# Performance work log

Hardware: AMD Instinct MI355X
Metric: run time of the kernel (lower is better)

Reference implementation:

```python
import jax, jax.numpy as jnp
import numpy as np

B, T, C = 4, 1024, 1024
N_HEAD = 16
MEMORY = 64  # sliding-window size: key j visible to query i iff 0 <= i-j <= MEMORY


def setup_inputs() -> dict:
    key = jax.random.key(0)
    k1, k2, k3 = jax.random.split(key, 3)
    x = jax.random.normal(k1, (B, T, C), dtype=jnp.float32)
    # torch Linear weight is [out, in]; we store transposed [in, out] for x @ W
    W_attn = jax.random.normal(k2, (C, 3 * C), dtype=jnp.float32) * (1.0 / np.sqrt(C))
    W_proj = jax.random.normal(k3, (C, C), dtype=jnp.float32) * (1.0 / np.sqrt(C))
    return {"x": x, "W_attn": W_attn, "W_proj": W_proj}


def reference(x, W_attn, W_proj):
    Bv, Tv, Cv = x.shape
    hd = Cv // N_HEAD
    qkv = x @ W_attn                               # [B,T,3C]
    q, k, v = jnp.split(qkv, 3, axis=-1)
    def heads(t):
        return t.reshape(Bv, Tv, N_HEAD, hd).transpose(0, 2, 1, 3)  # [B,H,T,hd]
    q, k, v = heads(q), heads(k), heads(v)
    scale = 1.0 / np.sqrt(hd)
    scores = jnp.einsum('bhqd,bhkd->bhqk', q, k) * scale            # [B,H,T,T]
    i = jnp.arange(Tv)
    diff = i[:, None] - i[None, :]                                  # i - j
    band_mask = (diff >= 0) & (diff <= MEMORY)                      # M1 * ~M2
    y = jax.nn.softmax(jnp.where(band_mask, scores, -jnp.inf), axis=-1) @ v
    # get_att=True path: full causal attention probabilities (no window)
    att = jax.nn.softmax(jnp.where(diff >= 0, scores, -jnp.inf), axis=-1)
    att_std = jnp.std(att, axis=0, ddof=1)                          # torch .std default ddof=1
    y = y.transpose(0, 2, 1, 3).reshape(Bv, Tv, Cv)
    y = y @ W_proj
    return (y, att, att_std)
```

## Files before the change

### kernel.cpp

```cpp
#include <hip/hip_runtime.h>
#include <hip/hip_bf16.h>
#include <stdint.h>

#define Bb 4
#define Tt 1024
#define Hh 16
#define HD 64
#define C3 3072
#define WIN 64

typedef __bf16 bf16x8 __attribute__((ext_vector_type(8)));
typedef float f32x4 __attribute__((ext_vector_type(4)));

#define MFMA16(a, b, c) __builtin_amdgcn_mfma_f32_16x16x32_bf16((a), (b), (c), 0, 0, 0)

static __device__ __forceinline__ unsigned short f2bf(float f) {
  union { float f; unsigned u; } v; v.f = f;
  unsigned r = (v.u + 0x7FFFu + ((v.u >> 16) & 1u)) >> 16;
  return (unsigned short)r;
}
static __device__ __forceinline__ float bf2f(unsigned short h) {
  union { unsigned u; float f; } v; v.u = ((unsigned)h) << 16;
  return v.f;
}

__global__ __launch_bounds__(256) void k_prep(const float* __restrict__ x,
                                              const float* __restrict__ Wa,
                                              const float* __restrict__ Wp,
                                              unsigned short* __restrict__ xbf,
                                              unsigned short* __restrict__ WtA,
                                              unsigned short* __restrict__ WtP) {
  __shared__ float tile[32][33];
  const int blk = blockIdx.x;
  const int tid = threadIdx.x;
  if (blk < 4096) {
    int i = blk * 256 + tid;
    float4 v = ((const float4*)x)[i];
    ushort4 o;
    o.x = f2bf(v.x); o.y = f2bf(v.y); o.z = f2bf(v.z); o.w = f2bf(v.w);
    ((ushort4*)xbf)[i] = o;
    return;
  }
  const float* Win; unsigned short* Wt; int N, n0, k0;
  if (blk < 7168) { int bb = blk - 4096; Win = Wa; Wt = WtA; N = 3072; n0 = (bb % 96) * 32; k0 = (bb / 96) * 32; }
  else           { int bb = blk - 7168; Win = Wp; Wt = WtP; N = 1024; n0 = (bb % 32) * 32; k0 = (bb / 32) * 32; }
  const int K = 1024;
  int tx = tid & 31, ty = tid >> 5;
  for (int r = ty; r < 32; r += 8)
    tile[r][tx] = Win[(size_t)(k0 + r) * N + n0 + tx];
  __syncthreads();
  for (int r = ty; r < 32; r += 8)
    Wt[(size_t)(n0 + r) * K + k0 + tx] = f2bf(tile[tx][r]);
}

template <int BM, int BF16_OUT, int SCALEQ>
__global__ __launch_bounds__(256) void k_gemm_bt(const unsigned short* __restrict__ A,
                                                 const unsigned short* __restrict__ Bt,
                                                 void* __restrict__ Cv, int M, int N, int K) {
  constexpr int MI = BM / 32;
  __shared__ unsigned short lds[BM * 32 + 128 * 32];
  unsigned short* as_ = lds;
  unsigned short* bs_ = lds + BM * 32;
  const int tid = threadIdx.x;
  const int m0 = blockIdx.x * BM, n0 = blockIdx.y * 128;
  const int w = tid >> 6, lane = tid & 63;
  const int wm = (w >> 1) * (BM / 2), wn = (w & 1) * 64;
  const int lrow = lane & 15, lk = lane >> 4;

  f32x4 z = {0.f, 0.f, 0.f, 0.f};
  f32x4 acc[MI][4];
#pragma unroll
  for (int i = 0; i < MI; ++i)
#pragma unroll
    for (int j = 0; j < 4; ++j) acc[i][j] = z;

  const int nk = K >> 5;
  for (int kt = 0; kt < nk; ++kt) {
    const int k0 = kt << 5;
    __syncthreads();
#pragma unroll
    for (int p = 0; p < BM / 64; ++p) {
      int seg = tid + p * 256;
      int row = seg >> 2, ks = (seg & 3) << 3;
      __builtin_amdgcn_global_load_lds(
          (__attribute__((address_space(1))) void*)(A + (size_t)(m0 + row) * K + k0 + ks),
          (__attribute__((address_space(3))) void*)(as_ + seg * 8), 16, 0, 0);
    }
#pragma unroll
    for (int p = 0; p < 2; ++p) {
      int seg = tid + p * 256;
      int row = seg >> 2, ks = (seg & 3) << 3;
      __builtin_amdgcn_global_load_lds(
          (__attribute__((address_space(1))) void*)(Bt + (size_t)(n0 + row) * K + k0 + ks),
          (__attribute__((address_space(3))) void*)(bs_ + seg * 8), 16, 0, 0);
    }
    __syncthreads();
    bf16x8 af[MI], bfr[4];
#pragma unroll
    for (int f = 0; f < MI; ++f)
      af[f] = *(const bf16x8*)(as_ + (wm + f * 16 + lrow) * 32 + lk * 8);
#pragma unroll
    for (int f = 0; f < 4; ++f)
      bfr[f] = *(const bf16x8*)(bs_ + (wn + f * 16 + lrow) * 32 + lk * 8);
#pragma unroll
    for (int i = 0; i < MI; ++i)
#pragma unroll
      for (int j = 0; j < 4; ++j) acc[i][j] = MFMA16(af[i], bfr[j], acc[i][j]);
  }
  const int r0 = lk * 4;
#pragma unroll
  for (int i = 0; i < MI; ++i)
#pragma unroll
    for (int j = 0; j < 4; ++j)
#pragma unroll
      for (int r = 0; r < 4; ++r) {
        int gm = m0 + wm + i * 16 + r0 + r;
        int gn = n0 + wn + j * 16 + lrow;
        float v = acc[i][j][r];
        if (SCALEQ) {
          if (gn < 1024) v *= 0.125f;
        }
        if (BF16_OUT)
          ((unsigned short*)Cv)[(size_t)gm * N + gn] = f2bf(v);
        else
          ((float*)Cv)[(size_t)gm * N + gn] = v;
      }
}

__global__ __launch_bounds__(256) void k_att(const unsigned short* __restrict__ qkv,
                                             float* __restrict__ att, float* __restrict__ astd) {
  const int ti = 31 - blockIdx.x;
  const int h = blockIdx.y;
  const int i0 = ti * 32;
  const int tid = threadIdx.x;
  const int w = tid >> 6, lane = tid & 63;
  const int lrow = lane & 15, lk = lane >> 4;

  __shared__ float smr[4][32][2];
  __shared__ float wbuf[4][32][36];

  {
    const int b1 = w;
    const size_t qb_ = ((size_t)(b1 * Tt + i0 + lrow)) * C3 + h * 64 + lk * 8;
    bf16x8 q00 = *(const bf16x8*)(qkv + qb_);
    bf16x8 q01 = *(const bf16x8*)(qkv + qb_ + 32);
    bf16x8 q10 = *(const bf16x8*)(qkv + qb_ + (size_t)16 * C3);
    bf16x8 q11 = *(const bf16x8*)(qkv + qb_ + (size_t)16 * C3 + 32);

    float m[2][4], l[2][4];
#pragma unroll
    for (int i2 = 0; i2 < 2; ++i2)
#pragma unroll
      for (int r = 0; r < 4; ++r) { m[i2][r] = -1e30f; l[i2][r] = 0.f; }

    for (int jt = 0; jt <= ti; ++jt) {
      const int j0 = jt * 32;
      const size_t krowa = ((size_t)(b1 * Tt + j0 + lrow)) * C3 + 1024 + h * 64 + lk * 8;
      const size_t krowb = krowa + (size_t)16 * C3;
      bf16x8 k00 = *(const bf16x8*)(qkv + krowa);
      bf16x8 k01 = *(const bf16x8*)(qkv + krowa + 32);
      bf16x8 k10 = *(const bf16x8*)(qkv + krowb);
      bf16x8 k11 = *(const bf16x8*)(qkv + krowb + 32);
      const int ja = j0 + lrow, jb2 = j0 + 16 + lrow;
#pragma unroll
      for (int i2 = 0; i2 < 2; ++i2) {
        bf16x8 qa = i2 ? q10 : q00;
        bf16x8 qb = i2 ? q11 : q01;
        f32x4 sa = {0.f, 0.f, 0.f, 0.f}, sb = {0.f, 0.f, 0.f, 0.f};
        sa = MFMA16(qa, k00, sa);
        sa = MFMA16(qb, k01, sa);
        sb = MFMA16(qa, k10, sb);
        sb = MFMA16(qb, k11, sb);
#pragma unroll
        for (int r = 0; r < 4; ++r) {
          int ig = i0 + i2 * 16 + lk * 4 + r;
          int oka = (ja <= ig), okb = (jb2 <= ig);
          float va = oka ? sa[r] : -1e30f;
          float vb = okb ? sb[r] : -1e30f;
          float mn = fmaxf(m[i2][r], fmaxf(va, vb));
          float pa = oka ? __expf(sa[r] - mn) : 0.f;
          float pb = okb ? __expf(sb[r] - mn) : 0.f;
          l[i2][r] = l[i2][r] * __expf(m[i2][r] - mn) + pa + pb;
          m[i2][r] = mn;
        }
      }
    }
#pragma unroll
    for (int i2 = 0; i2 < 2; ++i2)
#pragma unroll
      for (int r = 0; r < 4; ++r) {
        float mm = m[i2][r], ll = l[i2][r];
#pragma unroll
        for (int d = 1; d <= 8; d <<= 1) {
          float mo = __shfl_xor(mm, d);
          float lo = __shfl_xor(ll, d);
          float mn = fmaxf(mm, mo);
          ll = ll * __expf(mm - mn) + lo * __expf(mo - mn);
          mm = mn;
        }
        if (lrow == 0) {
          int row = i2 * 16 + lk * 4 + r;
          smr[b1][row][0] = mm;
          smr[b1][row][1] = 1.0f / ll;
        }
      }
  }
  __syncthreads();

  bf16x8 qf[4][2][2];
#pragma unroll
  for (int b = 0; b < 4; ++b) {
    const size_t qb_ = ((size_t)(b * Tt + i0 + lrow)) * C3 + h * 64 + lk * 8;
    qf[b][0][0] = *(const bf16x8*)(qkv + qb_);
    qf[b][0][1] = *(const bf16x8*)(qkv + qb_ + 32);
    qf[b][1][0] = *(const bf16x8*)(qkv + qb_ + (size_t)16 * C3);
    qf[b][1][1] = *(const bf16x8*)(qkv + qb_ + (size_t)16 * C3 + 32);
  }

  const float4 z4 = make_float4(0.f, 0.f, 0.f, 0.f);
  for (int jt = w; jt < 32; jt += 4) {
    const int j0 = jt * 32;
    if (jt > ti) {
#pragma unroll
      for (int b = 0; b < 4; ++b)
#pragma unroll
        for (int q = 0; q < 4; ++q) {
          int f = q * 64 + lane;
          int row = f >> 3, c4 = f & 7;
          *(float4*)&att[(((size_t)(b * Hh + h)) * Tt + i0 + row) * Tt + j0 + c4 * 4] = z4;
        }
#pragma unroll
      for (int q = 0; q < 4; ++q) {
        int f = q * 64 + lane;
        int row = f >> 3, c4 = f & 7;
        *(float4*)&astd[((size_t)h * Tt + i0 + row) * Tt + j0 + c4 * 4] = z4;
      }
      continue;
    }
    float s1[2][2][4], s2[2][2][4];
#pragma unroll
    for (int i2 = 0; i2 < 2; ++i2)
#pragma unroll
      for (int j2 = 0; j2 < 2; ++j2)
#pragma unroll
        for (int r = 0; r < 4; ++r) { s1[i2][j2][r] = 0.f; s2[i2][j2][r] = 0.f; }

#pragma unroll
    for (int b = 0; b < 4; ++b) {
      const size_t krowa = ((size_t)(b * Tt + j0 + lrow)) * C3 + 1024 + h * 64 + lk * 8;
      const size_t krowb = krowa + (size_t)16 * C3;
      bf16x8 k00 = *(const bf16x8*)(qkv + krowa);
      bf16x8 k01 = *(const bf16x8*)(qkv + krowa + 32);
      bf16x8 k10 = *(const bf16x8*)(qkv + krowb);
      bf16x8 k11 = *(const bf16x8*)(qkv + krowb + 32);
#pragma unroll
      for (int i2 = 0; i2 < 2; ++i2) {
        float mm[4], rr[4];
#pragma unroll
        for (int r = 0; r < 4; ++r) {
          int row = i2 * 16 + lk * 4 + r;
          mm[r] = smr[b][row][0];
          rr[r] = smr[b][row][1];
        }
#pragma unroll
        for (int j2 = 0; j2 < 2; ++j2) {
          f32x4 s = {0.f, 0.f, 0.f, 0.f};
          s = MFMA16(qf[b][i2][0], j2 ? k10 : k00, s);
          s = MFMA16(qf[b][i2][1], j2 ? k11 : k01, s);
          const int jg2 = j0 + j2 * 16 + lrow;
#pragma unroll
          for (int r = 0; r < 4; ++r) {
            int ig = i0 + i2 * 16 + lk * 4 + r;
            float p = (jg2 <= ig) ? __expf(s[r] - mm[r]) * rr[r] : 0.f;
            wbuf[w][i2 * 16 + lk * 4 + r][j2 * 16 + lrow] = p;
            s1[i2][j2][r] += p;
            s2[i2][j2][r] += p * p;
          }
        }
      }
#pragma unroll
      for (int q = 0; q < 4; ++q) {
        int f = q * 64 + lane;
        int row = f >> 3, c4 = f & 7;
        float4 v = *(float4*)&wbuf[w][row][c4 * 4];
        *(float4*)&att[(((size_t)(b * Hh + h)) * Tt + i0 + row) * Tt + j0 + c4 * 4] = v;
      }
    }
#pragma unroll
    for (int i2 = 0; i2 < 2; ++i2)
#pragma unroll
      for (int j2 = 0; j2 < 2; ++j2)
#pragma unroll
        for (int r = 0; r < 4; ++r) {
          float mean = s1[i2][j2][r] * 0.25f;
          float var = (s2[i2][j2][r] - 4.f * mean * mean) * (1.f / 3.f);
          wbuf[w][i2 * 16 + lk * 4 + r][j2 * 16 + lrow] = sqrtf(fmaxf(var, 0.f));
        }
#pragma unroll
    for (int q = 0; q < 4; ++q) {
      int f = q * 64 + lane;
      int row = f >> 3, c4 = f & 7;
      float4 v = *(float4*)&wbuf[w][row][c4 * 4];
      *(float4*)&astd[((size_t)h * Tt + i0 + row) * Tt + j0 + c4 * 4] = v;
    }
  }
}

__global__ __launch_bounds__(256) void k_bandy(const unsigned short* __restrict__ qkv,
                                               unsigned short* __restrict__ yh) {
  __shared__ unsigned short qls[64 * 66];
  __shared__ unsigned short kls[128 * 66];
  __shared__ unsigned short vls[128 * 66];
  __shared__ float pls[4][80];

  int blk = blockIdx.x;
  int it = blk & 15, h = (blk >> 4) & 15, b = blk >> 8;
  int i0 = it * 64;
  int jb = i0 - 64;
  int tid = threadIdx.x;

  for (int r = tid; r < 320; r += 256) {
    unsigned short* dst;
    int grow, sel;
    if (r < 64) { dst = qls + r * 66; grow = i0 + r; sel = 0; }
    else if (r < 192) { dst = kls + (r - 64) * 66; grow = jb + (r - 64); sel = 1; }
    else { dst = vls + (r - 192) * 66; grow = jb + (r - 192); sel = 2; }
    if (grow < 0) {
      for (int t = 0; t < 32; ++t) ((unsigned*)dst)[t] = 0u;
    } else {
      const unsigned* src = (const unsigned*)(qkv + ((size_t)(b * Tt + grow)) * C3 + sel * 1024 + h * 64);
      for (int t = 0; t < 32; ++t) ((unsigned*)dst)[t] = src[t];
    }
  }
  __syncthreads();

  const int w = tid >> 6, lane = tid & 63;
  for (int rr = 0; rr < 16; ++rr) {
    const int i = i0 + (w << 4) + rr;
    const int io = i - i0;
    const int ja = i - 64 + lane;
    const unsigned* qrow = (const unsigned*)(qls + io * 66);
    const unsigned* krow = (const unsigned*)(kls + (size_t)(io + lane) * 66);
    const unsigned* kerow = (const unsigned*)(kls + (size_t)(io + 64) * 66);
    float sa = 0.f, se = 0.f;
#pragma unroll 8
    for (int t = 0; t < 32; ++t) {
      unsigned qq = qrow[t];
      float q0 = bf2f((unsigned short)qq), q1 = bf2f((unsigned short)(qq >> 16));
      unsigned kk = krow[t];
      sa = fmaf(q0, bf2f((unsigned short)kk), sa);
      sa = fmaf(q1, bf2f((unsigned short)(kk >> 16)), sa);
      unsigned ke = kerow[t];
      se = fmaf(q0, bf2f((unsigned short)ke), se);
      se = fmaf(q1, bf2f((unsigned short)(ke >> 16)), se);
    }
    if (ja < 0) sa = -1e30f;
    float m = sa;
    m = fmaxf(m, __shfl_xor(m, 1));
    m = fmaxf(m, __shfl_xor(m, 2));
    m = fmaxf(m, __shfl_xor(m, 4));
    m = fmaxf(m, __shfl_xor(m, 8));
    m = fmaxf(m, __shfl_xor(m, 16));
    m = fmaxf(m, __shfl_xor(m, 32));
    m = fmaxf(m, se);
    float pa = __expf(sa - m);
    float pe = __expf(se - m);
    float sum = pa;
    sum += __shfl_xor(sum, 1);
    sum += __shfl_xor(sum, 2);
    sum += __shfl_xor(sum, 4);
    sum += __shfl_xor(sum, 8);
    sum += __shfl_xor(sum, 16);
    sum += __shfl_xor(sum, 32);
    sum += pe;
    float rl = 1.0f / sum;
    pls[w][lane] = pa * rl;
    if (lane == 0) pls[w][64] = pe * rl;
    float y = 0.f;
#pragma unroll 4
    for (int t = 0; t <= 64; ++t)
      y = fmaf(pls[w][t], bf2f(vls[(size_t)(io + t) * 66 + lane]), y);
    yh[((size_t)(b * Tt + i)) * 1024 + h * 64 + lane] = f2bf(y);
  }
}

extern "C" void kernel_launch(void* const* d_in, const int* in_sizes, int n_in,
                              void* d_out, int out_size, void* d_ws, size_t ws_size,
                              hipStream_t stream) {
  const float* x = (const float*)d_in[0];
  const float* Wa = (const float*)d_in[1];
  const float* Wp = (const float*)d_in[2];

  float* out = (float*)d_out;
  float* y_out = out;
  float* att = out + (size_t)4194304;
  float* astd = out + (size_t)71303168;

  char* ws = (char*)d_ws;
  unsigned short* qkv = (unsigned short*)ws;
  unsigned short* yh = (unsigned short*)(ws + 25165824);
  unsigned short* WtP = (unsigned short*)(ws + 33554432);

  char* yreg = (char*)d_out;
  unsigned short* WtA = (unsigned short*)yreg;
  unsigned short* xbf = (unsigned short*)(yreg + 6291456);

  k_prep<<<8192, 256, 0, stream>>>(x, Wa, Wp, xbf, WtA, WtP);
  k_gemm_bt<128, 1, 1><<<dim3(32, 24), 256, 0, stream>>>(xbf, WtA, qkv, 4096, 3072, 1024);
  k_att<<<dim3(32, 16), 256, 0, stream>>>(qkv, att, astd);
  k_bandy<<<1024, 256, 0, stream>>>(qkv, yh);
  k_gemm_bt<64, 0, 0><<<dim3(64, 8), 256, 0, stream>>>(yh, WtP, y_out, 4096, 1024, 1024);
}
```

Measured before the change: 293.0 us.

## Merge causal-attention and band-attention kernels into one interleaved launch

Combines the full causal attention probability/std kernel and the sliding-window band attention kernel into a single launch. Block IDs are interleaved so that one of every three blocks does causal-attention work and the other two do band work, letting the two independent workloads share the GPU at the same time. The intent is to fill idle compute units during the imbalanced, memory-heavy att kernel and to remove one launch boundary. The cost is a shared memory allocation sized to the larger of the two paths, which can lower occupancy for the band blocks, and a divergent kernel body that may increase register pressure.

```diff
diff --git a/kernel.cpp b/kernel.cpp
--- a/kernel.cpp
+++ b/kernel.cpp
@@ -127,260 +127,264 @@
       }
 }
 
-__global__ __launch_bounds__(256) void k_att(const unsigned short* __restrict__ qkv,
-                                             float* __restrict__ att, float* __restrict__ astd) {
-  const int ti = 31 - blockIdx.x;
-  const int h = blockIdx.y;
-  const int i0 = ti * 32;
+__global__ __launch_bounds__(256) void k_attband(const unsigned short* __restrict__ qkv,
+                                                 float* __restrict__ att, float* __restrict__ astd,
+                                                 unsigned short* __restrict__ yh) {
+  __shared__ __align__(16) char smem[43520];
+  const int bid = blockIdx.x;
+  const int g = bid / 3, rsel = bid - g * 3;
   const int tid = threadIdx.x;
   const int w = tid >> 6, lane = tid & 63;
-  const int lrow = lane & 15, lk = lane >> 4;
-
-  __shared__ float smr[4][32][2];
-  __shared__ float wbuf[4][32][36];
-
-  {
-    const int b1 = w;
-    const size_t qb_ = ((size_t)(b1 * Tt + i0 + lrow)) * C3 + h * 64 + lk * 8;
-    bf16x8 q00 = *(const bf16x8*)(qkv + qb_);
-    bf16x8 q01 = *(const bf16x8*)(qkv + qb_ + 32);
-    bf16x8 q10 = *(const bf16x8*)(qkv + qb_ + (size_t)16 * C3);
-    bf16x8 q11 = *(const bf16x8*)(qkv + qb_ + (size_t)16 * C3 + 32);
-
-    float m[2][4], l[2][4];
-#pragma unroll
-    for (int i2 = 0; i2 < 2; ++i2)
-#pragma unroll
-      for (int r = 0; r < 4; ++r) { m[i2][r] = -1e30f; l[i2][r] = 0.f; }
-
-    for (int jt = 0; jt <= ti; ++jt) {
+
+  if (rsel == 0) {
+    const int ti = 31 - (g & 31);
+    const int h = g >> 5;
+    const int i0 = ti * 32;
+    const int lrow = lane & 15, lk = lane >> 4;
+    float (*smr)[32][2] = (float(*)[32][2])smem;
+    float (*wbuf)[32][36] = (float(*)[32][36])(smem + 1024);
+
+    {
+      const int b1 = w;
+      const size_t qb_ = ((size_t)(b1 * Tt + i0 + lrow)) * C3 + h * 64 + lk * 8;
+      bf16x8 q00 = *(const bf16x8*)(qkv + qb_);
+      bf16x8 q01 = *(const bf16x8*)(qkv + qb_ + 32);
+      bf16x8 q10 = *(const bf16x8*)(qkv + qb_ + (size_t)16 * C3);
+      bf16x8 q11 = *(const bf16x8*)(qkv + qb_ + (size_t)16 * C3 + 32);
+
+      float m[2][4], l[2][4];
+#pragma unroll
+      for (int i2 = 0; i2 < 2; ++i2)
+#pragma unroll
+        for (int r = 0; r < 4; ++r) { m[i2][r] = -1e30f; l[i2][r] = 0.f; }
+
+      for (int jt = 0; jt <= ti; ++jt) {
+        const int j0 = jt * 32;
+        const size_t krowa = ((size_t)(b1 * Tt + j0 + lrow)) * C3 + 1024 + h * 64 + lk * 8;
+        const size_t krowb = krowa + (size_t)16 * C3;
+        bf16x8 k00 = *(const bf16x8*)(qkv + krowa);
+        bf16x8 k01 = *(const bf16x8*)(qkv + krowa + 32);
+        bf16x8 k10 = *(const bf16x8*)(qkv + krowb);
+        bf16x8 k11 = *(const bf16x8*)(qkv + krowb + 32);
+        const int ja = j0 + lrow, jb2 = j0 + 16 + lrow;
+#pragma unroll
+        for (int i2 = 0; i2 < 2; ++i2) {
+          bf16x8 qa = i2 ? q10 : q00;
+          bf16x8 qb = i2 ? q11 : q01;
+          f32x4 sa = {0.f, 0.f, 0.f, 0.f}, sb = {0.f, 0.f, 0.f, 0.f};
+          sa = MFMA16(qa, k00, sa);
+          sa = MFMA16(qb, k01, sa);
+          sb = MFMA16(qa, k10, sb);
+          sb = MFMA16(qb, k11, sb);
+#pragma unroll
+          for (int r = 0; r < 4; ++r) {
+            int ig = i0 + i2 * 16 + lk * 4 + r;
+            int oka = (ja <= ig), okb = (jb2 <= ig);
+            float va = oka ? sa[r] : -1e30f;
+            float vb = okb ? sb[r] : -1e30f;
+            float mn = fmaxf(m[i2][r], fmaxf(va, vb));
+            float pa = oka ? __expf(sa[r] - mn) : 0.f;
+            float pb = okb ? __expf(sb[r] - mn) : 0.f;
+            l[i2][r] = l[i2][r] * __expf(m[i2][r] - mn) + pa + pb;
+            m[i2][r] = mn;
+          }
+        }
+      }
+#pragma unroll
+      for (int i2 = 0; i2 < 2; ++i2)
+#pragma unroll
+        for (int r = 0; r < 4; ++r) {
+          float mm = m[i2][r], ll = l[i2][r];
+#pragma unroll
+          for (int d = 1; d <= 8; d <<= 1) {
+            float mo = __shfl_xor(mm, d);
+            float lo = __shfl_xor(ll, d);
+            float mn = fmaxf(mm, mo);
+            ll = ll * __expf(mm - mn) + lo * __expf(mo - mn);
+            mm = mn;
+          }
+          if (lrow == 0) {
+            int row = i2 * 16 + lk * 4 + r;
+            smr[b1][row][0] = mm;
+            smr[b1][row][1] = 1.0f / ll;
+          }
+        }
+    }
+    __syncthreads();
+
+    bf16x8 qf[4][2][2];
+#pragma unroll
+    for (int b = 0; b < 4; ++b) {
+      const size_t qb_ = ((size_t)(b * Tt + i0 + lrow)) * C3 + h * 64 + lk * 8;
+      qf[b][0][0] = *(const bf16x8*)(qkv + qb_);
+      qf[b][0][1] = *(const bf16x8*)(qkv + qb_ + 32);
+      qf[b][1][0] = *(const bf16x8*)(qkv + qb_ + (size_t)16 * C3);
+      qf[b][1][1] = *(const bf16x8*)(qkv + qb_ + (size_t)16 * C3 + 32);
+    }
+
+    const float4 z4 = make_float4(0.f, 0.f, 0.f, 0.f);
+    for (int jt = w; jt < 32; jt += 4) {
       const int j0 = jt * 32;
-      const size_t krowa = ((size_t)(b1 * Tt + j0 + lrow)) * C3 + 1024 + h * 64 + lk * 8;
-      const size_t krowb = krowa + (size_t)16 * C3;
-      bf16x8 k00 = *(const bf16x8*)(qkv + krowa);
-      bf16x8 k01 = *(const bf16x8*)(qkv + krowa + 32);
-      bf16x8 k10 = *(const bf16x8*)(qkv + krowb);
-      bf16x8 k11 = *(const bf16x8*)(qkv + krowb + 32);
-      const int ja = j0 + lrow, jb2 = j0 + 16 + lrow;
-#pragma unroll
-      for (int i2 = 0; i2 < 2; ++i2) {
-        bf16x8 qa = i2 ? q10 : q00;
-        bf16x8 qb = i2 ? q11 : q01;
-        f32x4 sa = {0.f, 0.f, 0.f, 0.f}, sb = {0.f, 0.f, 0.f, 0.f};
-        sa = MFMA16(qa, k00, sa);
-        sa = MFMA16(qb, k01, sa);
-        sb = MFMA16(qa, k10, sb);
-        sb = MFMA16(qb, k11, sb);
-#pragma unroll
-        for (int r = 0; r < 4; ++r) {
-          int ig = i0 + i2 * 16 + lk * 4 + r;
-          int oka = (ja <= ig), okb = (jb2 <= ig);
-          float va = oka ? sa[r] : -1e30f;
-          float vb = okb ? sb[r] : -1e30f;
-          float mn = fmaxf(m[i2][r], fmaxf(va, vb));
-          float pa = oka ? __expf(sa[r] - mn) : 0.f;
-          float pb = okb ? __expf(sb[r] - mn) : 0.f;
-          l[i2][r] = l[i2][r] * __expf(m[i2][r] - mn) + pa + pb;
-          m[i2][r] = mn;
-        }
-      }
-    }
-#pragma unroll
-    for (int i2 = 0; i2 < 2; ++i2)
-#pragma unroll
-      for (int r = 0; r < 4; ++r) {
-        float mm = m[i2][r], ll = l[i2][r];
-#pragma unroll
-        for (int d = 1; d <= 8; d <<= 1) {
-          float mo = __shfl_xor(mm, d);
-          float lo = __shfl_xor(ll, d);
-          float mn = fmaxf(mm, mo);
-          ll = ll * __expf(mm - mn) + lo * __expf(mo - mn);
-          mm = mn;
-        }
-        if (lrow == 0) {
-          int row = i2 * 16 + lk * 4 + r;
-          smr[b1][row][0] = mm;
-          smr[b1][row][1] = 1.0f / ll;
-        }
-      }
-  }
-  __syncthreads();
-
-  bf16x8 qf[4][2][2];
-#pragma unroll
-  for (int b = 0; b < 4; ++b) {
-    const size_t qb_ = ((size_t)(b * Tt + i0 + lrow)) * C3 + h * 64 + lk * 8;
-    qf[b][0][0] = *(const bf16x8*)(qkv + qb_);
-    qf[b][0][1] = *(const bf16x8*)(qkv + qb_ + 32);
-    qf[b][1][0] = *(const bf16x8*)(qkv + qb_ + (size_t)16 * C3);
-    qf[b][1][1] = *(const bf16x8*)(qkv + qb_ + (size_t)16 * C3 + 32);
-  }
-
-  const float4 z4 = make_float4(0.f, 0.f, 0.f, 0.f);
-  for (int jt = w; jt < 32; jt += 4) {
-    const int j0 = jt * 32;
-    if (jt > ti) {
-#pragma unroll
-      for (int b = 0; b < 4; ++b)
+      if (jt > ti) {
+#pragma unroll
+        for (int b = 0; b < 4; ++b)
+#pragma unroll
+          for (int q = 0; q < 4; ++q) {
+            int f = q * 64 + lane;
+            int row = f >> 3, c4 = f & 7;
+            *(float4*)&att[(((size_t)(b * Hh + h)) * Tt + i0 + row) * Tt + j0 + c4 * 4] = z4;
+          }
 #pragma unroll
         for (int q = 0; q < 4; ++q) {
           int f = q * 64 + lane;
           int row = f >> 3, c4 = f & 7;
-          *(float4*)&att[(((size_t)(b * Hh + h)) * Tt + i0 + row) * Tt + j0 + c4 * 4] = z4;
-        }
-#pragma unroll
-      for (int q = 0; q < 4; ++q) {
-        int f = q * 64 + lane;
-        int row = f >> 3, c4 = f & 7;
-        *(float4*)&astd[((size_t)h * Tt + i0 + row) * Tt + j0 + c4 * 4] = z4;
-      }
-      continue;
-    }
-    float s1[2][2][4], s2[2][2][4];
-#pragma unroll
-    for (int i2 = 0; i2 < 2; ++i2)
-#pragma unroll
-      for (int j2 = 0; j2 < 2; ++j2)
-#pragma unroll
-        for (int r = 0; r < 4; ++r) { s1[i2][j2][r] = 0.f; s2[i2][j2][r] = 0.f; }
-
-#pragma unroll
-    for (int b = 0; b < 4; ++b) {
-      const size_t krowa = ((size_t)(b * Tt + j0 + lrow)) * C3 + 1024 + h * 64 + lk * 8;
-      const size_t krowb = krowa + (size_t)16 * C3;
-      bf16x8 k00 = *(const bf16x8*)(qkv + krowa);
-      bf16x8 k01 = *(const bf16x8*)(qkv + krowa + 32);
-      bf16x8 k10 = *(const bf16x8*)(qkv + krowb);
-      bf16x8 k11 = *(const bf16x8*)(qkv + krowb + 32);
-#pragma unroll
-      for (int i2 = 0; i2 < 2; ++i2) {
-        float mm[4], rr[4];
-#pragma unroll
-        for (int r = 0; r < 4; ++r) {
-          int row = i2 * 16 + lk * 4 + r;
-          mm[r] = smr[b][row][0];
-          rr[r] = smr[b][row][1];
-        }
-#pragma unroll
-        for (int j2 = 0; j2 < 2; ++j2) {
-          f32x4 s = {0.f, 0.f, 0.f, 0.f};
-          s = MFMA16(qf[b][i2][0], j2 ? k10 : k00, s);
-          s = MFMA16(qf[b][i2][1], j2 ? k11 : k01, s);
-          const int jg2 = j0 + j2 * 16 + lrow;
+          *(float4*)&astd[((size_t)h * Tt + i0 + row) * Tt + j0 + c4 * 4] = z4;
+        }
+        continue;
+      }
+      float s1[2][2][4], s2[2][2][4];
+#pragma unroll
+      for (int i2 = 0; i2 < 2; ++i2)
+#pragma unroll
+        for (int j2 = 0; j2 < 2; ++j2)
+#pragma unroll
+          for (int r = 0; r < 4; ++r) { s1[i2][j2][r] = 0.f; s2[i2][j2][r] = 0.f; }
+
+#pragma unroll
+      for (int b = 0; b < 4; ++b) {
+        const size_t krowa = ((size_t)(b * Tt + j0 + lrow)) * C3 + 1024 + h * 64 + lk * 8;
+        const size_t krowb = krowa + (size_t)16 * C3;
+        bf16x8 k00 = *(const bf16x8*)(qkv + krowa);
+        bf16x8 k01 = *(const bf16x8*)(qkv + krowa + 32);
+        bf16x8 k10 = *(const bf16x8*)(qkv + krowb);
+        bf16x8 k11 = *(const bf16x8*)(qkv + krowb + 32);
+#pragma unroll
+        for (int i2 = 0; i2 < 2; ++i2) {
+          float mm[4], rr[4];
 #pragma unroll
           for (int r = 0; r < 4; ++r) {
-            int ig = i0 + i2 * 16 + lk * 4 + r;
-            float p = (jg2 <= ig) ? __expf(s[r] - mm[r]) * rr[r] : 0.f;
-            wbuf[w][i2 * 16 + lk * 4 + r][j2 * 16 + lrow] = p;
-            s1[i2][j2][r] += p;
-            s2[i2][j2][r] += p * p;
-          }
-        }
-      }
+            int row = i2 * 16 + lk * 4 + r;
+            mm[r] = smr[b][row][0];
+            rr[r] = smr[b][row][1];
+          }
+#pragma unroll
+          for (int j2 = 0; j2 < 2; ++j2) {
+            f32x4 s = {0.f, 0.f, 0.f, 0.f};
+            s = MFMA16(qf[b][i2][0], j2 ? k10 : k00, s);
+            s = MFMA16(qf[b][i2][1], j2 ? k11 : k01, s);
+            const int jg2 = j0 + j2 * 16 + lrow;
+#pragma unroll
+            for (int r = 0; r < 4; ++r) {
+              int ig = i0 + i2 * 16 + lk * 4 + r;
+              float p = (jg2 <= ig) ? __expf(s[r] - mm[r]) * rr[r] : 0.f;
+              wbuf[w][i2 * 16 + lk * 4 + r][j2 * 16 + lrow] = p;
+              s1[i2][j2][r] += p;
+              s2[i2][j2][r] += p * p;
+            }
+          }
+        }
+#pragma unroll
+        for (int q = 0; q < 4; ++q) {
+          int f = q * 64 + lane;
+          int row = f >> 3, c4 = f & 7;
+          float4 v = *(float4*)&wbuf[w][row][c4 * 4];
+          *(float4*)&att[(((size_t)(b * Hh + h)) * Tt + i0 + row) * Tt + j0 + c4 * 4] = v;
+        }
+      }
+#pragma unroll
+      for (int i2 = 0; i2 < 2; ++i2)
+#pragma unroll
+        for (int j2 = 0; j2 < 2; ++j2)
+#pragma unroll
+          for (int r = 0; r < 4; ++r) {
+            float mean = s1[i2][j2][r] * 0.25f;
+            float var = (s2[i2][j2][r] - 4.f * mean * mean) * (1.f / 3.f);
+            wbuf[w][i2 * 16 + lk * 4 + r][j2 * 16 + lrow] = sqrtf(fmaxf(var, 0.f));
+          }
 #pragma unroll
       for (int q = 0; q < 4; ++q) {
         int f = q * 64 + lane;
         int row = f >> 3, c4 = f & 7;
         float4 v = *(float4*)&wbuf[w][row][c4 * 4];
-        *(float4*)&att[(((size_t)(b * Hh + h)) * Tt + i0 + row) * Tt + j0 + c4 * 4] = v;
-      }
-    }
-#pragma unroll
-    for (int i2 = 0; i2 < 2; ++i2)
-#pragma unroll
-      for (int j2 = 0; j2 < 2; ++j2)
-#pragma unroll
-        for (int r = 0; r < 4; ++r) {
-          float mean = s1[i2][j2][r] * 0.25f;
-          float var = (s2[i2][j2][r] - 4.f * mean * mean) * (1.f / 3.f);
-          wbuf[w][i2 * 16 + lk * 4 + r][j2 * 16 + lrow] = sqrtf(fmaxf(var, 0.f));
-        }
-#pragma unroll
-    for (int q = 0; q < 4; ++q) {
-      int f = q * 64 + lane;
-      int row = f >> 3, c4 = f & 7;
-      float4 v = *(float4*)&wbuf[w][row][c4 * 4];
-      *(float4*)&astd[((size_t)h * Tt + i0 + row) * Tt + j0 + c4 * 4] = v;
-    }
+        *(float4*)&astd[((size_t)h * Tt + i0 + row) * Tt + j0 + c4 * 4] = v;
+      }
+    }
+    return;
   }
-}
-
-__global__ __launch_bounds__(256) void k_bandy(const unsigned short* __restrict__ qkv,
-                                               unsigned short* __restrict__ yh) {
-  __shared__ unsigned short qls[64 * 66];
-  __shared__ unsigned short kls[128 * 66];
-  __shared__ unsigned short vls[128 * 66];
-  __shared__ float pls[4][80];
-
-  int blk = blockIdx.x;
-  int it = blk & 15, h = (blk >> 4) & 15, b = blk >> 8;
-  int i0 = it * 64;
-  int jb = i0 - 64;
-  int tid = threadIdx.x;
-
-  for (int r = tid; r < 320; r += 256) {
-    unsigned short* dst;
-    int grow, sel;
-    if (r < 64) { dst = qls + r * 66; grow = i0 + r; sel = 0; }
-    else if (r < 192) { dst = kls + (r - 64) * 66; grow = jb + (r - 64); sel = 1; }
-    else { dst = vls + (r - 192) * 66; grow = jb + (r - 192); sel = 2; }
-    if (grow < 0) {
-      for (int t = 0; t < 32; ++t) ((unsigned*)dst)[t] = 0u;
-    } else {
-      const unsigned* src = (const unsigned*)(qkv + ((size_t)(b * Tt + grow)) * C3 + sel * 1024 + h * 64);
-      for (int t = 0; t < 32; ++t) ((unsigned*)dst)[t] = src[t];
-    }
-  }
-  __syncthreads();
-
-  const int w = tid >> 6, lane = tid & 63;
-  for (int rr = 0; rr < 16; ++rr) {
-    const int i = i0 + (w << 4) + rr;
-    const int io = i - i0;
-    const int ja = i - 64 + lane;
-    const unsigned* qrow = (const unsigned*)(qls + io * 66);
-    const unsigned* krow = (const unsigned*)(kls + (size_t)(io + lane) * 66);
-    const unsigned* kerow = (const unsigned*)(kls + (size_t)(io + 64) * 66);
-    float sa = 0.f, se = 0.f;
+
+  {
+    const int blk = 2 * g + (rsel - 1);
+    unsigned short* qls = (unsigned short*)smem;
+    unsigned short* kls = qls + 64 * 66;
+    unsigned short* vls = kls + 128 * 66;
+    float (*pls)[80] = (float(*)[80])(smem + (64 + 128 + 128) * 66 * 2);
+
+    int it = blk & 15, h = (blk >> 4) & 15, b = blk >> 8;
+    int i0 = it * 64;
+    int jb = i0 - 64;
+
+    for (int r = tid; r < 320; r += 256) {
+      unsigned short* dst;
+      int grow, sel;
+      if (r < 64) { dst = qls + r * 66; grow = i0 + r; sel = 0; }
+      else if (r < 192) { dst = kls + (r - 64) * 66; grow = jb + (r - 64); sel = 1; }
+      else { dst = vls + (r - 192) * 66; grow = jb + (r - 192); sel = 2; }
+      if (grow < 0) {
+        for (int t = 0; t < 32; ++t) ((unsigned*)dst)[t] = 0u;
+      } else {
+        const unsigned* src = (const unsigned*)(qkv + ((size_t)(b * Tt + grow)) * C3 + sel * 1024 + h * 64);
+        for (int t = 0; t < 32; ++t) ((unsigned*)dst)[t] = src[t];
+      }
+    }
+    __syncthreads();
+
+    for (int rr = 0; rr < 16; ++rr) {
+      const int i = i0 + (w << 4) + rr;
+      const int io = i - i0;
+      const int ja = i - 64 + lane;
+      const unsigned* qrow = (const unsigned*)(qls + io * 66);
+      const unsigned* krow = (const unsigned*)(kls + (size_t)(io + lane) * 66);
+      const unsigned* kerow = (const unsigned*)(kls + (size_t)(io + 64) * 66);
+      float sa = 0.f, se = 0.f;
 #pragma unroll 8
-    for (int t = 0; t < 32; ++t) {
-      unsigned qq = qrow[t];
-      float q0 = bf2f((unsigned short)qq), q1 = bf2f((unsigned short)(qq >> 16));
-      unsigned kk = krow[t];
-      sa = fmaf(q0, bf2f((unsigned short)kk), sa);
-      sa = fmaf(q1, bf2f((unsigned short)(kk >> 16)), sa);
-      unsigned ke = kerow[t];
-      se = fmaf(q0, bf2f((unsigned short)ke), se);
-      se = fmaf(q1, bf2f((unsigned short)(ke >> 16)), se);
-    }
-    if (ja < 0) sa = -1e30f;
-    float m = sa;
-    m = fmaxf(m, __shfl_xor(m, 1));
-    m = fmaxf(m, __shfl_xor(m, 2));
-    m = fmaxf(m, __shfl_xor(m, 4));
-    m = fmaxf(m, __shfl_xor(m, 8));
-    m = fmaxf(m, __shfl_xor(m, 16));
-    m = fmaxf(m, __shfl_xor(m, 32));
-    m = fmaxf(m, se);
-    float pa = __expf(sa - m);
-    float pe = __expf(se - m);
-    float sum = pa;
-    sum += __shfl_xor(sum, 1);
-    sum += __shfl_xor(sum, 2);
-    sum += __shfl_xor(sum, 4);
-    sum += __shfl_xor(sum, 8);
-    sum += __shfl_xor(sum, 16);
-    sum += __shfl_xor(sum, 32);
-    sum += pe;
-    float rl = 1.0f / sum;
-    pls[w][lane] = pa * rl;
-    if (lane == 0) pls[w][64] = pe * rl;
-    float y = 0.f;
+      for (int t = 0; t < 32; ++t) {
+        unsigned qq = qrow[t];
+        float q0 = bf2f((unsigned short)qq), q1 = bf2f((unsigned short)(qq >> 16));
+        unsigned kk = krow[t];
+        sa = fmaf(q0, bf2f((unsigned short)kk), sa);
+        sa = fmaf(q1, bf2f((unsigned short)(kk >> 16)), sa);
+        unsigned ke = kerow[t];
+        se = fmaf(q0, bf2f((unsigned short)ke), se);
+        se = fmaf(q1, bf2f((unsigned short)(ke >> 16)), se);
+      }
+      if (ja < 0) sa = -1e30f;
+      float m = sa;
+      m = fmaxf(m, __shfl_xor(m, 1));
+      m = fmaxf(m, __shfl_xor(m, 2));
+      m = fmaxf(m, __shfl_xor(m, 4));
+      m = fmaxf(m, __shfl_xor(m, 8));
+      m = fmaxf(m, __shfl_xor(m, 16));
+      m = fmaxf(m, __shfl_xor(m, 32));
+      m = fmaxf(m, se);
+      float pa = __expf(sa - m);
+      float pe = __expf(se - m);
+      float sum = pa;
+      sum += __shfl_xor(sum, 1);
+      sum += __shfl_xor(sum, 2);
+      sum += __shfl_xor(sum, 4);
+      sum += __shfl_xor(sum, 8);
+      sum += __shfl_xor(sum, 16);
+      sum += __shfl_xor(sum, 32);
+      sum += pe;
+      float rl = 1.0f / sum;
+      pls[w][lane] = pa * rl;
+      if (lane == 0) pls[w][64] = pe * rl;
+      float y = 0.f;
 #pragma unroll 4
-    for (int t = 0; t <= 64; ++t)
-      y = fmaf(pls[w][t], bf2f(vls[(size_t)(io + t) * 66 + lane]), y);
-    yh[((size_t)(b * Tt + i)) * 1024 + h * 64 + lane] = f2bf(y);
+      for (int t = 0; t <= 64; ++t)
+        y = fmaf(pls[w][t], bf2f(vls[(size_t)(io + t) * 66 + lane]), y);
+      yh[((size_t)(b * Tt + i)) * 1024 + h * 64 + lane] = f2bf(y);
+    }
   }
 }
 
@@ -407,7 +411,6 @@
 
   k_prep<<<8192, 256, 0, stream>>>(x, Wa, Wp, xbf, WtA, WtP);
   k_gemm_bt<128, 1, 1><<<dim3(32, 24), 256, 0, stream>>>(xbf, WtA, qkv, 4096, 3072, 1024);
-  k_att<<<dim3(32, 16), 256, 0, stream>>>(qkv, att, astd);
-  k_bandy<<<1024, 256, 0, stream>>>(qkv, yh);
+  k_attband<<<1536, 256, 0, stream>>>(qkv, att, astd, yh);
   k_gemm_bt<64, 0, 0><<<dim3(64, 8), 256, 0, stream>>>(yh, WtP, y_out, 4096, 1024, 1024);
 }
```

After: 306.0 us. 1.04x slower.
